# Kernel optimization log

Measured on AMD Instinct MI355X. Metric: run time of the kernel, lower is better.

Reference implementation:

```python
import jax, jax.numpy as jnp
import numpy as np

N = 50000      # nodes
E = 800000     # edges (before self-loops)
F_IN = 128     # in_dim
H = 8          # heads
C = 16         # out_dim per head
NEG_SLOPE = 0.2
EPS = 1e-5


def setup_inputs() -> dict:
    key = jax.random.key(0)
    ks = jax.random.split(key, 8)
    x = jax.random.normal(ks[0], (N, F_IN), dtype=jnp.float32)
    edge_index = jax.random.randint(ks[1], (2, E), 0, N, dtype=jnp.int64)
    # GAT linear weight (xavier-ish scale), stored as [F_IN, H*C]
    W_gat = jax.random.normal(ks[2], (F_IN, H * C), dtype=jnp.float32) * 0.1
    att_src = jax.random.normal(ks[3], (H, C), dtype=jnp.float32) * 0.1
    att_dst = jax.random.normal(ks[4], (H, C), dtype=jnp.float32) * 0.1
    bias_gat = jnp.zeros((H * C,), dtype=jnp.float32)
    W_skip = jax.random.normal(ks[5], (F_IN, H * C), dtype=jnp.float32) * 0.1
    gamma = jnp.ones((H * C,), dtype=jnp.float32)
    beta = jnp.zeros((H * C,), dtype=jnp.float32)
    return {"x": x, "edge_index": edge_index, "W_gat": W_gat,
            "att_src": att_src, "att_dst": att_dst, "bias_gat": bias_gat,
            "W_skip": W_skip, "gamma": gamma, "beta": beta}


def reference(x, edge_index, W_gat, att_src, att_dst, bias_gat, W_skip, gamma, beta):
    # PyG GATConv default: add self-loops
    loop = jnp.arange(N, dtype=edge_index.dtype)
    src = jnp.concatenate([edge_index[0], loop])  # [E+N]
    dst = jnp.concatenate([edge_index[1], loop])  # [E+N]

    h = (x @ W_gat).reshape(N, H, C)              # [N,H,C]
    a_src = jnp.sum(h * att_src, axis=-1)          # [N,H]
    a_dst = jnp.sum(h * att_dst, axis=-1)          # [N,H]

    e = jax.nn.leaky_relu(a_src[src] + a_dst[dst], NEG_SLOPE)   # [E+N,H]
    # segment softmax over destination nodes
    e_max = jax.ops.segment_max(e, dst, num_segments=N)         # [N,H]
    e_exp = jnp.exp(e - e_max[dst])
    denom = jax.ops.segment_sum(e_exp, dst, num_segments=N)     # [N,H]
    alpha = e_exp / denom[dst]                                   # [E+N,H]

    msg = alpha[:, :, None] * h[src]                             # [E+N,H,C]
    gat_out = jax.ops.segment_sum(msg, dst, num_segments=N)     # [N,H,C]
    gat_out = gat_out.reshape(N, H * C) + bias_gat

    skip_out = x @ W_skip                                        # [N,H*C]
    z = gat_out + 0.1 * skip_out

    mu = jnp.mean(z, axis=-1, keepdims=True)
    var = jnp.mean((z - mu) ** 2, axis=-1, keepdims=True)
    z = (z - mu) * jax.lax.rsqrt(var + EPS) * gamma + beta
    return jax.nn.elu(z)  # dropout is identity in eval mode
```

## Files before the change

kernel.cpp:

```cpp
#include <hip/hip_runtime.h>
#include <hip/hip_bf16.h>

#define N_NODES 50000
#define N_EDGES 800000
#define F_IN    128
#define HC      128
#define NR      8
#define RSZ     6250
#define NCH     16
#define CHSZ    50000
#define NP      50048

typedef __attribute__((ext_vector_type(8))) short bf16x8;
typedef __attribute__((ext_vector_type(4))) float f32x4;

__device__ __forceinline__ float bf2f(unsigned int u16) {
    return __uint_as_float(u16 << 16);
}
__device__ __forceinline__ unsigned int f2bf(float f) {
    unsigned int u = __float_as_uint(f);
    return (u + 0x7fffu + ((u >> 16) & 1u)) >> 16;
}

__global__ __launch_bounds__(256) void k_hist(
    const int* __restrict__ dst,
    const float* __restrict__ Wg, const float* __restrict__ Ws,
    unsigned short* __restrict__ Bfrag, int* __restrict__ part)
{
    const int bid = blockIdx.x;
    const int tid = threadIdx.x;
    if (bid < 128) {
        __shared__ int hist[RSZ];
        const int r = bid & 7, c = bid >> 3;
        const int nb = r * RSZ;
        for (int i = tid; i < RSZ; i += 256) hist[i] = 0;
        __syncthreads();
        const int4* d4 = (const int4*)(dst + c * CHSZ);
        for (int i = tid; i < CHSZ / 4; i += 256) {
            const int4 v = d4[i];
            int b;
            b = v.x - nb; if ((unsigned)b < (unsigned)RSZ) atomicAdd(&hist[b], 1);
            b = v.y - nb; if ((unsigned)b < (unsigned)RSZ) atomicAdd(&hist[b], 1);
            b = v.z - nb; if ((unsigned)b < (unsigned)RSZ) atomicAdd(&hist[b], 1);
            b = v.w - nb; if ((unsigned)b < (unsigned)RSZ) atomicAdd(&hist[b], 1);
        }
        __syncthreads();
        for (int i = tid; i < RSZ; i += 256)
            part[(size_t)c * NP + nb + i] = hist[i];
    } else {
        const int g = (bid - 128) * 256 + tid;
        if (g < 4096) {
            const int lane = g & 63;
            const int kq = (g >> 6) & 3;
            const int nt = g >> 8;
            const int cc = nt * 16 + (lane & 15);
            const int kbase = kq * 32 + (lane >> 4) * 8;
            const float* Wsel = (cc < 128) ? (Wg + cc) : (Ws + cc - 128);
            unsigned int pk[4];
#pragma unroll
            for (int p = 0; p < 4; p++) {
                const float v0 = Wsel[(size_t)(kbase + 2 * p) * HC];
                const float v1 = Wsel[(size_t)(kbase + 2 * p + 1) * HC];
                pk[p] = f2bf(v0) | (f2bf(v1) << 16);
            }
            *(uint4*)(Bfrag + (size_t)g * 8) = make_uint4(pk[0], pk[1], pk[2], pk[3]);
        }
    }
}

__global__ __launch_bounds__(256) void k_scanA(
    int* __restrict__ part, int* __restrict__ counts,
    int* __restrict__ row_start, int* __restrict__ bsum)
{
    __shared__ int s[256];
    const int tid = threadIdx.x;
    const int base = blockIdx.x * 1024 + tid * 4;
    int v[4]; int t = 0;
#pragma unroll
    for (int j = 0; j < 4; j++) {
        const int idx = base + j;
        if (idx < N_NODES) {
            int run = 0;
#pragma unroll
            for (int c = 0; c < 16; c++) {
                int* p = part + (size_t)c * NP + idx;
                const int q = *p;
                *p = run;
                run += q;
            }
            counts[idx] = run;
            v[j] = run + 1;
        } else v[j] = 0;
        t += v[j];
    }
    s[tid] = t;
    __syncthreads();
    for (int off = 1; off < 256; off <<= 1) {
        int add = (tid >= off) ? s[tid - off] : 0;
        __syncthreads();
        s[tid] += add;
        __syncthreads();
    }
    int excl = s[tid] - t;
#pragma unroll
    for (int j = 0; j < 4; j++) {
        const int idx = base + j;
        if (idx < N_NODES) row_start[idx] = excl;
        excl += v[j];
    }
    if (tid == 255) bsum[blockIdx.x] = s[255];
}

__global__ __launch_bounds__(256) void k_scanC(
    int* __restrict__ row_start, const int* __restrict__ bsum,
    const int* __restrict__ counts, int* __restrict__ csr)
{
    __shared__ int soff;
    const int tid = threadIdx.x;
    if (tid < 64) {
        const int tgt = blockIdx.x >> 2;
        int v = (tid < 49 && tid < tgt) ? bsum[tid] : 0;
#pragma unroll
        for (int off = 1; off < 64; off <<= 1) v += __shfl_xor(v, off);
        if (tid == 0) soff = v;
    }
    __syncthreads();
    const int i = blockIdx.x * 256 + tid;
    if (i < N_NODES) {
        const int rs = row_start[i] + soff;
        row_start[i] = rs;
        csr[rs + counts[i]] = i;
    }
}

__global__ __launch_bounds__(256) void k_lf(
    const float* __restrict__ x,
    const unsigned short* __restrict__ Bfrag,
    const float* __restrict__ att_s,
    const float* __restrict__ att_d,
    const float* __restrict__ bias,
    unsigned short* __restrict__ h_bf, unsigned int* __restrict__ z0b,
    float* __restrict__ a_src, float* __restrict__ a_dst,
    const int* __restrict__ src, const int* __restrict__ dst,
    const int* __restrict__ row_start, const int* __restrict__ part,
    int* __restrict__ csr)
{
    __shared__ __align__(16) int smem[RSZ];
    const int bid = blockIdx.x;
    const int tid = threadIdx.x;
    int lin = -1, r = 0, c = 0;
    if (bid < 256) {
        const int g = bid >> 4, pos = bid & 15;
        if (pos < 8) { r = pos; c = g; }
        else lin = g * 8 + (pos - 8);
    } else {
        lin = 128 + (bid - 256);
    }

    if (lin < 0) {
        const int nb = r * RSZ;
        for (int b = tid; b < RSZ; b += 256)
            smem[b] = row_start[nb + b] + part[(size_t)c * NP + nb + b];
        __syncthreads();
        const int4* d4 = (const int4*)(dst + c * CHSZ);
        const int4* s4 = (const int4*)(src + c * CHSZ);
        for (int i = tid; i < CHSZ / 4; i += 256) {
            const int4 dv = d4[i];
            const int4 sv = s4[i];
            int b;
            b = dv.x - nb; if ((unsigned)b < (unsigned)RSZ) csr[atomicAdd(&smem[b], 1)] = sv.x;
            b = dv.y - nb; if ((unsigned)b < (unsigned)RSZ) csr[atomicAdd(&smem[b], 1)] = sv.y;
            b = dv.z - nb; if ((unsigned)b < (unsigned)RSZ) csr[atomicAdd(&smem[b], 1)] = sv.z;
            b = dv.w - nb; if ((unsigned)b < (unsigned)RSZ) csr[atomicAdd(&smem[b], 1)] = sv.w;
        }
        return;
    }

    unsigned short* sA = (unsigned short*)smem;
    const int lane = tid & 63;
    const int w = tid >> 6;
    const int nbase = lin * 64;

#pragma unroll
    for (int it = 0; it < 4; it++) {
        const int p = it * 256 + tid;
        const int node = p >> 4;
        const int kg = p & 15;
        const int gn = nbase + node;
        float v[8];
        if (gn < N_NODES) {
            float4 u0 = *(const float4*)(x + (size_t)gn * F_IN + kg * 8);
            float4 u1 = *(const float4*)(x + (size_t)gn * F_IN + kg * 8 + 4);
            v[0] = u0.x; v[1] = u0.y; v[2] = u0.z; v[3] = u0.w;
            v[4] = u1.x; v[5] = u1.y; v[6] = u1.z; v[7] = u1.w;
        } else {
#pragma unroll
            for (int j = 0; j < 8; j++) v[j] = 0.f;
        }
        const int mt = node >> 4, lm = node & 15;
        const int kq = kg >> 2, quad = kg & 3;
        uint4 pk;
        pk.x = f2bf(v[0]) | (f2bf(v[1]) << 16);
        pk.y = f2bf(v[2]) | (f2bf(v[3]) << 16);
        pk.z = f2bf(v[4]) | (f2bf(v[5]) << 16);
        pk.w = f2bf(v[6]) | (f2bf(v[7]) << 16);
        *(uint4*)(sA + ((size_t)((mt * 4 + kq) * 64 + quad * 16 + lm)) * 8) = pk;
    }
    __syncthreads();

    const bf16x8* Bf = (const bf16x8*)Bfrag;
    f32x4 acc[4][4];
#pragma unroll
    for (int mt = 0; mt < 4; mt++)
#pragma unroll
        for (int nt = 0; nt < 4; nt++)
            acc[mt][nt] = (f32x4){0.f, 0.f, 0.f, 0.f};

#pragma unroll
    for (int kq = 0; kq < 4; kq++) {
        bf16x8 aF[4], bF[4];
#pragma unroll
        for (int nt = 0; nt < 4; nt++)
            bF[nt] = Bf[(size_t)(((w * 4 + nt) * 4 + kq) * 64 + lane)];
#pragma unroll
        for (int mt = 0; mt < 4; mt++)
            aF[mt] = *(const bf16x8*)(sA + ((size_t)((mt * 4 + kq) * 64 + lane)) * 8);
#pragma unroll
        for (int mt = 0; mt < 4; mt++)
#pragma unroll
            for (int nt = 0; nt < 4; nt++)
                acc[mt][nt] = __builtin_amdgcn_mfma_f32_16x16x32_bf16(
                    aF[mt], bF[nt], acc[mt][nt], 0, 0, 0);
    }

    __syncthreads();

    const int row4 = (lane >> 4) * 4;
    const int cl = lane & 15;
    unsigned int* hls = (unsigned int*)smem;

    if (w < 2) {
#pragma unroll
        for (int mt = 0; mt < 4; mt++) {
#pragma unroll
            for (int nt = 0; nt < 4; nt++) {
                const int cc = w * 64 + nt * 16 + cl;
                f32x4 d = acc[mt][nt];
#pragma unroll
                for (int rr = 0; rr < 4; rr++) {
                    const float oth = __shfl_xor(d[rr], 1);
                    if ((cl & 1) == 0) {
                        const int nl = mt * 16 + row4 + rr;
                        hls[nl * 68 + (cc >> 1)] = f2bf(d[rr]) | (f2bf(oth) << 16);
                    }
                }
            }
        }
    } else {
#pragma unroll
        for (int mt = 0; mt < 4; mt++) {
#pragma unroll
            for (int nt = 0; nt < 4; nt++) {
                const int cz = (w - 2) * 64 + nt * 16 + cl;
                f32x4 d = acc[mt][nt];
                const float bv = bias[cz];
#pragma unroll
                for (int rr = 0; rr < 4; rr++) {
                    const int gn = nbase + mt * 16 + row4 + rr;
                    const float val = 0.1f * d[rr] + bv;
                    const float oth = __shfl_xor(val, 1);
                    if ((cl & 1) == 0 && gn < N_NODES)
                        z0b[(size_t)gn * 64 + (cz >> 1)] = f2bf(val) | (f2bf(oth) << 16);
                }
            }
        }
    }
    __syncthreads();

    {
        const int row = tid >> 2, q = tid & 3;
        const int gn = nbase + row;
        if (gn < N_NODES) {
            const unsigned int* hr = hls + row * 68 + q * 16;
            uint4 v0 = *(const uint4*)(hr);
            uint4 v1 = *(const uint4*)(hr + 4);
            uint4 v2 = *(const uint4*)(hr + 8);
            uint4 v3 = *(const uint4*)(hr + 12);
            uint4* hout = (uint4*)((unsigned int*)h_bf + (size_t)gn * 64 + q * 16);
            hout[0] = v0; hout[1] = v1; hout[2] = v2; hout[3] = v3;

            const unsigned int u[16] = {v0.x, v0.y, v0.z, v0.w,
                                        v1.x, v1.y, v1.z, v1.w,
                                        v2.x, v2.y, v2.z, v2.w,
                                        v3.x, v3.y, v3.z, v3.w};
            const int c0 = q * 32;
            const float4* as4 = (const float4*)(att_s + c0);
            const float4* ad4 = (const float4*)(att_d + c0);
            float ds0 = 0.f, dd0 = 0.f, ds1 = 0.f, dd1 = 0.f;
#pragma unroll
            for (int j = 0; j < 4; j++) {
                const float4 sa = as4[j], da = ad4[j];
                float l0 = bf2f(u[2 * j] & 0xffffu),     h0v = bf2f(u[2 * j] >> 16);
                float l1 = bf2f(u[2 * j + 1] & 0xffffu), h1v = bf2f(u[2 * j + 1] >> 16);
                ds0 += l0 * sa.x + h0v * sa.y + l1 * sa.z + h1v * sa.w;
                dd0 += l0 * da.x + h0v * da.y + l1 * da.z + h1v * da.w;
                const float4 sb = as4[4 + j], db = ad4[4 + j];
                float l2 = bf2f(u[8 + 2 * j] & 0xffffu),     h2v = bf2f(u[8 + 2 * j] >> 16);
                float l3 = bf2f(u[8 + 2 * j + 1] & 0xffffu), h3v = bf2f(u[8 + 2 * j + 1] >> 16);
                ds1 += l2 * sb.x + h2v * sb.y + l3 * sb.z + h3v * sb.w;
                dd1 += l2 * db.x + h2v * db.y + l3 * db.z + h3v * db.w;
            }
            const int hh = 2 * q;
            a_src[gn * 8 + hh] = ds0;     a_src[gn * 8 + hh + 1] = ds1;
            a_dst[gn * 8 + hh] = dd0;     a_dst[gn * 8 + hh + 1] = dd1;
        }
    }
}

__global__ __launch_bounds__(256) void k_agg(
    const unsigned int* __restrict__ h32,
    const unsigned int* __restrict__ z0b,
    const float* __restrict__ a_src, const float* __restrict__ a_dst,
    const int* __restrict__ row_start, const int* __restrict__ counts,
    const int* __restrict__ csr,
    const float* __restrict__ gamma, const float* __restrict__ beta,
    float* __restrict__ out)
{
    const int tid = threadIdx.x;
    const int lane = tid & 63;
    const int n = blockIdx.x * 4 + (tid >> 6);
    const int head = lane >> 3;

    const float adn = a_dst[n * 8 + head];
    const int rs  = __builtin_amdgcn_readfirstlane(row_start[n]);
    const int cnt = __builtin_amdgcn_readfirstlane(counts[n]) + 1;

    float d_acc = 0.f, a0 = 0.f, a1 = 0.f;
    for (int i = 0; i < cnt; i += 8) {
        int s[8]; float ae[8], mk[8]; unsigned int hp[8];
#pragma unroll
        for (int j = 0; j < 8; j++) {
            const int e = i + j;
            const int ec = (e < cnt) ? e : (cnt - 1);
            mk[j] = (e < cnt) ? 1.f : 0.f;
            s[j] = csr[rs + ec];
        }
#pragma unroll
        for (int j = 0; j < 8; j++) ae[j] = a_src[s[j] * 8 + head];
#pragma unroll
        for (int j = 0; j < 8; j++) hp[j] = h32[(size_t)s[j] * 64 + lane];
#pragma unroll
        for (int j = 0; j < 8; j++) {
            float e = ae[j] + adn;
            e = (e > 0.f) ? e : 0.2f * e;
            const float wgt = __expf(e) * mk[j];
            d_acc += wgt;
            a0 += wgt * bf2f(hp[j] & 0xffffu);
            a1 += wgt * bf2f(hp[j] >> 16);
        }
    }
    const float inv = 1.0f / d_acc;
    const unsigned int zp = z0b[(size_t)n * 64 + lane];
    float y0 = a0 * inv + bf2f(zp & 0xffffu);
    float y1 = a1 * inv + bf2f(zp >> 16);

    float ss = y0 + y1;
#pragma unroll
    for (int off = 1; off < 64; off <<= 1) ss += __shfl_xor(ss, off);
    const float mu = ss * (1.0f / 128.0f);
    const float d0 = y0 - mu, d1 = y1 - mu;
    float vs = d0 * d0 + d1 * d1;
#pragma unroll
    for (int off = 1; off < 64; off <<= 1) vs += __shfl_xor(vs, off);
    const float rstd = rsqrtf(vs * (1.0f / 128.0f) + 1e-5f);

    const float2 gv = *(const float2*)(gamma + lane * 2);
    const float2 bv = *(const float2*)(beta + lane * 2);
    float o0 = d0 * rstd * gv.x + bv.x;
    float o1 = d1 * rstd * gv.y + bv.y;
    o0 = (o0 > 0.f) ? o0 : (__expf(o0) - 1.0f);
    o1 = (o1 > 0.f) ? o1 : (__expf(o1) - 1.0f);

    *(float2*)(out + (size_t)n * HC + lane * 2) = make_float2(o0, o1);
}

extern "C" void kernel_launch(void* const* d_in, const int* in_sizes, int n_in,
                              void* d_out, int out_size, void* d_ws, size_t ws_size,
                              hipStream_t stream) {
    const float* x   = (const float*)d_in[0];
    const int*   ei  = (const int*)d_in[1];
    const float* Wg  = (const float*)d_in[2];
    const float* as_ = (const float*)d_in[3];
    const float* ad_ = (const float*)d_in[4];
    const float* bg  = (const float*)d_in[5];
    const float* Wsk = (const float*)d_in[6];
    const float* gm  = (const float*)d_in[7];
    const float* bt  = (const float*)d_in[8];
    float* out = (float*)d_out;

    char* wsb = (char*)d_ws;
    unsigned short* h_bf  = (unsigned short*)wsb;
    unsigned int*   z0b   = (unsigned int*)(wsb + 12800000);
    float*          a_src = (float*)(wsb + 25600000);
    float*          a_dst = (float*)(wsb + 27200000);
    unsigned short* Bfrag = (unsigned short*)(wsb + 28800000);
    int*   counts = (int*)(wsb + 28865536);
    int*   row_st = (int*)(wsb + 29065728);
    int*   bsum   = (int*)(wsb + 29265920);
    int*   csr    = (int*)(wsb + 29266944);
    int*   part   = (int*)(wsb + 32666944);

    const int* src = ei;
    const int* dst = ei + N_EDGES;

    k_hist <<<144, 256, 0, stream>>>(dst, Wg, Wsk, Bfrag, part);
    k_scanA<<<49, 256, 0, stream>>>(part, counts, row_st, bsum);
    k_scanC<<<196, 256, 0, stream>>>(row_st, bsum, counts, csr);
    k_lf   <<<910, 256, 0, stream>>>(x, Bfrag, as_, ad_, bg, h_bf, z0b,
                                     a_src, a_dst, src, dst, row_st, part, csr);
    k_agg  <<<N_NODES / 4, 256, 0, stream>>>((const unsigned int*)h_bf, z0b,
                                             a_src, a_dst, row_st, counts, csr,
                                             gm, bt, out);
}
```

Measured before the change: 213.1 us.

## Spread linear-projection blocks across histogram, scan and scatter kernels and double edge chunks

The dense linear projection (x times weights, attention logits) is moved out of a single kernel and split into three slices. Each slice is co-scheduled with one CSR-building stage: histogram, partial scan and scatter. This fills GPU idle time during those low-occupancy phases. The edge list is also cut into 32 chunks instead of 16, giving the histogram and scatter stages more blocks. The weight packing moves into its own small kernel, which adds one launch, and the scan now reads twice as many per-chunk partial counts.

```diff
diff --git a/kernel.cpp b/kernel.cpp
--- a/kernel.cpp
+++ b/kernel.cpp
@@ -7,8 +7,8 @@
 #define HC      128
 #define NR      8
 #define RSZ     6250
-#define NCH     16
-#define CHSZ    50000
+#define NCH     32
+#define CHSZ    25000
 #define NP      50048
 
 typedef __attribute__((ext_vector_type(8))) short bf16x8;
@@ -22,160 +22,14 @@
     return (u + 0x7fffu + ((u >> 16) & 1u)) >> 16;
 }
 
-__global__ __launch_bounds__(256) void k_hist(
-    const int* __restrict__ dst,
-    const float* __restrict__ Wg, const float* __restrict__ Ws,
-    unsigned short* __restrict__ Bfrag, int* __restrict__ part)
-{
-    const int bid = blockIdx.x;
-    const int tid = threadIdx.x;
-    if (bid < 128) {
-        __shared__ int hist[RSZ];
-        const int r = bid & 7, c = bid >> 3;
-        const int nb = r * RSZ;
-        for (int i = tid; i < RSZ; i += 256) hist[i] = 0;
-        __syncthreads();
-        const int4* d4 = (const int4*)(dst + c * CHSZ);
-        for (int i = tid; i < CHSZ / 4; i += 256) {
-            const int4 v = d4[i];
-            int b;
-            b = v.x - nb; if ((unsigned)b < (unsigned)RSZ) atomicAdd(&hist[b], 1);
-            b = v.y - nb; if ((unsigned)b < (unsigned)RSZ) atomicAdd(&hist[b], 1);
-            b = v.z - nb; if ((unsigned)b < (unsigned)RSZ) atomicAdd(&hist[b], 1);
-            b = v.w - nb; if ((unsigned)b < (unsigned)RSZ) atomicAdd(&hist[b], 1);
-        }
-        __syncthreads();
-        for (int i = tid; i < RSZ; i += 256)
-            part[(size_t)c * NP + nb + i] = hist[i];
-    } else {
-        const int g = (bid - 128) * 256 + tid;
-        if (g < 4096) {
-            const int lane = g & 63;
-            const int kq = (g >> 6) & 3;
-            const int nt = g >> 8;
-            const int cc = nt * 16 + (lane & 15);
-            const int kbase = kq * 32 + (lane >> 4) * 8;
-            const float* Wsel = (cc < 128) ? (Wg + cc) : (Ws + cc - 128);
-            unsigned int pk[4];
-#pragma unroll
-            for (int p = 0; p < 4; p++) {
-                const float v0 = Wsel[(size_t)(kbase + 2 * p) * HC];
-                const float v1 = Wsel[(size_t)(kbase + 2 * p + 1) * HC];
-                pk[p] = f2bf(v0) | (f2bf(v1) << 16);
-            }
-            *(uint4*)(Bfrag + (size_t)g * 8) = make_uint4(pk[0], pk[1], pk[2], pk[3]);
-        }
-    }
-}
-
-__global__ __launch_bounds__(256) void k_scanA(
-    int* __restrict__ part, int* __restrict__ counts,
-    int* __restrict__ row_start, int* __restrict__ bsum)
-{
-    __shared__ int s[256];
-    const int tid = threadIdx.x;
-    const int base = blockIdx.x * 1024 + tid * 4;
-    int v[4]; int t = 0;
-#pragma unroll
-    for (int j = 0; j < 4; j++) {
-        const int idx = base + j;
-        if (idx < N_NODES) {
-            int run = 0;
-#pragma unroll
-            for (int c = 0; c < 16; c++) {
-                int* p = part + (size_t)c * NP + idx;
-                const int q = *p;
-                *p = run;
-                run += q;
-            }
-            counts[idx] = run;
-            v[j] = run + 1;
-        } else v[j] = 0;
-        t += v[j];
-    }
-    s[tid] = t;
-    __syncthreads();
-    for (int off = 1; off < 256; off <<= 1) {
-        int add = (tid >= off) ? s[tid - off] : 0;
-        __syncthreads();
-        s[tid] += add;
-        __syncthreads();
-    }
-    int excl = s[tid] - t;
-#pragma unroll
-    for (int j = 0; j < 4; j++) {
-        const int idx = base + j;
-        if (idx < N_NODES) row_start[idx] = excl;
-        excl += v[j];
-    }
-    if (tid == 255) bsum[blockIdx.x] = s[255];
-}
-
-__global__ __launch_bounds__(256) void k_scanC(
-    int* __restrict__ row_start, const int* __restrict__ bsum,
-    const int* __restrict__ counts, int* __restrict__ csr)
-{
-    __shared__ int soff;
-    const int tid = threadIdx.x;
-    if (tid < 64) {
-        const int tgt = blockIdx.x >> 2;
-        int v = (tid < 49 && tid < tgt) ? bsum[tid] : 0;
-#pragma unroll
-        for (int off = 1; off < 64; off <<= 1) v += __shfl_xor(v, off);
-        if (tid == 0) soff = v;
-    }
-    __syncthreads();
-    const int i = blockIdx.x * 256 + tid;
-    if (i < N_NODES) {
-        const int rs = row_start[i] + soff;
-        row_start[i] = rs;
-        csr[rs + counts[i]] = i;
-    }
-}
-
-__global__ __launch_bounds__(256) void k_lf(
-    const float* __restrict__ x,
-    const unsigned short* __restrict__ Bfrag,
-    const float* __restrict__ att_s,
-    const float* __restrict__ att_d,
+__device__ __forceinline__ void linear_block(
+    int lin, int tid, int* smem,
+    const float* __restrict__ x, const unsigned short* __restrict__ Bfrag,
+    const float* __restrict__ att_s, const float* __restrict__ att_d,
     const float* __restrict__ bias,
     unsigned short* __restrict__ h_bf, unsigned int* __restrict__ z0b,
-    float* __restrict__ a_src, float* __restrict__ a_dst,
-    const int* __restrict__ src, const int* __restrict__ dst,
-    const int* __restrict__ row_start, const int* __restrict__ part,
-    int* __restrict__ csr)
-{
-    __shared__ __align__(16) int smem[RSZ];
-    const int bid = blockIdx.x;
-    const int tid = threadIdx.x;
-    int lin = -1, r = 0, c = 0;
-    if (bid < 256) {
-        const int g = bid >> 4, pos = bid & 15;
-        if (pos < 8) { r = pos; c = g; }
-        else lin = g * 8 + (pos - 8);
-    } else {
-        lin = 128 + (bid - 256);
-    }
-
-    if (lin < 0) {
-        const int nb = r * RSZ;
-        for (int b = tid; b < RSZ; b += 256)
-            smem[b] = row_start[nb + b] + part[(size_t)c * NP + nb + b];
-        __syncthreads();
-        const int4* d4 = (const int4*)(dst + c * CHSZ);
-        const int4* s4 = (const int4*)(src + c * CHSZ);
-        for (int i = tid; i < CHSZ / 4; i += 256) {
-            const int4 dv = d4[i];
-            const int4 sv = s4[i];
-            int b;
-            b = dv.x - nb; if ((unsigned)b < (unsigned)RSZ) csr[atomicAdd(&smem[b], 1)] = sv.x;
-            b = dv.y - nb; if ((unsigned)b < (unsigned)RSZ) csr[atomicAdd(&smem[b], 1)] = sv.y;
-            b = dv.z - nb; if ((unsigned)b < (unsigned)RSZ) csr[atomicAdd(&smem[b], 1)] = sv.z;
-            b = dv.w - nb; if ((unsigned)b < (unsigned)RSZ) csr[atomicAdd(&smem[b], 1)] = sv.w;
-        }
-        return;
-    }
-
+    float* __restrict__ a_src, float* __restrict__ a_dst)
+{
     unsigned short* sA = (unsigned short*)smem;
     const int lane = tid & 63;
     const int w = tid >> 6;
@@ -317,6 +171,183 @@
     }
 }
 
+__global__ __launch_bounds__(256) void k_pack(
+    const float* __restrict__ Wg, const float* __restrict__ Ws,
+    unsigned short* __restrict__ Bfrag)
+{
+    const int g = blockIdx.x * 256 + threadIdx.x;
+    if (g < 4096) {
+        const int lane = g & 63;
+        const int kq = (g >> 6) & 3;
+        const int nt = g >> 8;
+        const int cc = nt * 16 + (lane & 15);
+        const int kbase = kq * 32 + (lane >> 4) * 8;
+        const float* Wsel = (cc < 128) ? (Wg + cc) : (Ws + cc - 128);
+        unsigned int pk[4];
+#pragma unroll
+        for (int p = 0; p < 4; p++) {
+            const float v0 = Wsel[(size_t)(kbase + 2 * p) * HC];
+            const float v1 = Wsel[(size_t)(kbase + 2 * p + 1) * HC];
+            pk[p] = f2bf(v0) | (f2bf(v1) << 16);
+        }
+        *(uint4*)(Bfrag + (size_t)g * 8) = make_uint4(pk[0], pk[1], pk[2], pk[3]);
+    }
+}
+
+__global__ __launch_bounds__(256) void k_hl(
+    const int* __restrict__ dst, int* __restrict__ part,
+    const float* __restrict__ x, const unsigned short* __restrict__ Bfrag,
+    const float* __restrict__ att_s, const float* __restrict__ att_d,
+    const float* __restrict__ bias,
+    unsigned short* __restrict__ h_bf, unsigned int* __restrict__ z0b,
+    float* __restrict__ a_src, float* __restrict__ a_dst)
+{
+    __shared__ __align__(16) int smem[RSZ];
+    const int bid = blockIdx.x;
+    const int tid = threadIdx.x;
+    if (bid < 256) {
+        const int r = bid & 7, c = bid >> 3;
+        const int nb = r * RSZ;
+        for (int i = tid; i < RSZ; i += 256) smem[i] = 0;
+        __syncthreads();
+        const int4* d4 = (const int4*)(dst + c * CHSZ);
+        for (int i = tid; i < CHSZ / 4; i += 256) {
+            const int4 v = d4[i];
+            int b;
+            b = v.x - nb; if ((unsigned)b < (unsigned)RSZ) atomicAdd(&smem[b], 1);
+            b = v.y - nb; if ((unsigned)b < (unsigned)RSZ) atomicAdd(&smem[b], 1);
+            b = v.z - nb; if ((unsigned)b < (unsigned)RSZ) atomicAdd(&smem[b], 1);
+            b = v.w - nb; if ((unsigned)b < (unsigned)RSZ) atomicAdd(&smem[b], 1);
+        }
+        __syncthreads();
+        for (int i = tid; i < RSZ; i += 256)
+            part[(size_t)c * NP + nb + i] = smem[i];
+        return;
+    }
+    linear_block(bid - 256, tid, smem, x, Bfrag, att_s, att_d, bias,
+                 h_bf, z0b, a_src, a_dst);
+}
+
+__global__ __launch_bounds__(256) void k_sl(
+    int* __restrict__ part, int* __restrict__ counts,
+    int* __restrict__ row_start, int* __restrict__ bsum,
+    const float* __restrict__ x, const unsigned short* __restrict__ Bfrag,
+    const float* __restrict__ att_s, const float* __restrict__ att_d,
+    const float* __restrict__ bias,
+    unsigned short* __restrict__ h_bf, unsigned int* __restrict__ z0b,
+    float* __restrict__ a_src, float* __restrict__ a_dst)
+{
+    __shared__ __align__(16) int smem[RSZ];
+    const int bid = blockIdx.x;
+    const int tid = threadIdx.x;
+    if (bid < 49) {
+        int* s = smem;
+        const int base = bid * 1024 + tid * 4;
+        int v[4]; int t = 0;
+#pragma unroll
+        for (int j = 0; j < 4; j++) {
+            const int idx = base + j;
+            if (idx < N_NODES) {
+                int run = 0;
+#pragma unroll
+                for (int c = 0; c < NCH; c++) {
+                    int* p = part + (size_t)c * NP + idx;
+                    const int q = *p;
+                    *p = run;
+                    run += q;
+                }
+                counts[idx] = run;
+                v[j] = run + 1;
+            } else v[j] = 0;
+            t += v[j];
+        }
+        s[tid] = t;
+        __syncthreads();
+        for (int off = 1; off < 256; off <<= 1) {
+            int add = (tid >= off) ? s[tid - off] : 0;
+            __syncthreads();
+            s[tid] += add;
+            __syncthreads();
+        }
+        int excl = s[tid] - t;
+#pragma unroll
+        for (int j = 0; j < 4; j++) {
+            const int idx = base + j;
+            if (idx < N_NODES) row_start[idx] = excl;
+            excl += v[j];
+        }
+        if (tid == 255) bsum[bid] = s[255];
+        return;
+    }
+    linear_block(260 + (bid - 49), tid, smem, x, Bfrag, att_s, att_d, bias,
+                 h_bf, z0b, a_src, a_dst);
+}
+
+__global__ __launch_bounds__(256) void k_scanC(
+    int* __restrict__ row_start, const int* __restrict__ bsum,
+    const int* __restrict__ counts, int* __restrict__ csr)
+{
+    __shared__ int soff;
+    const int tid = threadIdx.x;
+    if (tid < 64) {
+        const int tgt = blockIdx.x >> 2;
+        int v = (tid < 49 && tid < tgt) ? bsum[tid] : 0;
+#pragma unroll
+        for (int off = 1; off < 64; off <<= 1) v += __shfl_xor(v, off);
+        if (tid == 0) soff = v;
+    }
+    __syncthreads();
+    const int i = blockIdx.x * 256 + tid;
+    if (i < N_NODES) {
+        const int rs = row_start[i] + soff;
+        row_start[i] = rs;
+        csr[rs + counts[i]] = i;
+    }
+}
+
+__global__ __launch_bounds__(256) void k_lf(
+    const int* __restrict__ src, const int* __restrict__ dst,
+    const int* __restrict__ row_start, const int* __restrict__ part,
+    int* __restrict__ csr,
+    const float* __restrict__ x, const unsigned short* __restrict__ Bfrag,
+    const float* __restrict__ att_s, const float* __restrict__ att_d,
+    const float* __restrict__ bias,
+    unsigned short* __restrict__ h_bf, unsigned int* __restrict__ z0b,
+    float* __restrict__ a_src, float* __restrict__ a_dst)
+{
+    __shared__ __align__(16) int smem[RSZ];
+    const int bid = blockIdx.x;
+    const int tid = threadIdx.x;
+    int lin;
+    if (bid < 512) {
+        const int c = bid >> 4, pos = bid & 15;
+        if (pos < 8) {
+            const int r = pos;
+            const int nb = r * RSZ;
+            for (int b = tid; b < RSZ; b += 256)
+                smem[b] = row_start[nb + b] + part[(size_t)c * NP + nb + b];
+            __syncthreads();
+            const int4* d4 = (const int4*)(dst + c * CHSZ);
+            const int4* s4 = (const int4*)(src + c * CHSZ);
+            for (int i = tid; i < CHSZ / 4; i += 256) {
+                const int4 dv = d4[i];
+                const int4 sv = s4[i];
+                int b;
+                b = dv.x - nb; if ((unsigned)b < (unsigned)RSZ) csr[atomicAdd(&smem[b], 1)] = sv.x;
+                b = dv.y - nb; if ((unsigned)b < (unsigned)RSZ) csr[atomicAdd(&smem[b], 1)] = sv.y;
+                b = dv.z - nb; if ((unsigned)b < (unsigned)RSZ) csr[atomicAdd(&smem[b], 1)] = sv.z;
+                b = dv.w - nb; if ((unsigned)b < (unsigned)RSZ) csr[atomicAdd(&smem[b], 1)] = sv.w;
+            }
+            return;
+        }
+        lin = 521 + c * 8 + (pos - 8);
+    } else {
+        lin = 777 + (bid - 512);
+    }
+    linear_block(lin, tid, smem, x, Bfrag, att_s, att_d, bias,
+                 h_bf, z0b, a_src, a_dst);
+}
+
 __global__ __launch_bounds__(256) void k_agg(
     const unsigned int* __restrict__ h32,
     const unsigned int* __restrict__ z0b,
@@ -413,11 +444,16 @@
     const int* src = ei;
     const int* dst = ei + N_EDGES;
 
-    k_hist <<<144, 256, 0, stream>>>(dst, Wg, Wsk, Bfrag, part);
-    k_scanA<<<49, 256, 0, stream>>>(part, counts, row_st, bsum);
+    k_pack <<<16, 256, 0, stream>>>(Wg, Wsk, Bfrag);
+    k_hl   <<<516, 256, 0, stream>>>(dst, part, x, Bfrag, as_, ad_, bg,
+                                     h_bf, z0b, a_src, a_dst);
+    k_sl   <<<310, 256, 0, stream>>>(part, counts, row_st, bsum,
+                                     x, Bfrag, as_, ad_, bg,
+                                     h_bf, z0b, a_src, a_dst);
     k_scanC<<<196, 256, 0, stream>>>(row_st, bsum, counts, csr);
-    k_lf   <<<910, 256, 0, stream>>>(x, Bfrag, as_, ad_, bg, h_bf, z0b,
-                                     a_src, a_dst, src, dst, row_st, part, csr);
+    k_lf   <<<517, 256, 0, stream>>>(src, dst, row_st, part, csr,
+                                     x, Bfrag, as_, ad_, bg,
+                                     h_bf, z0b, a_src, a_dst);
     k_agg  <<<N_NODES / 4, 256, 0, stream>>>((const unsigned int*)h_bf, z0b,
                                              a_src, a_dst, row_st, counts, csr,
                                              gm, bt, out);
```

Result: no change. 209.1 us (-1.9%).
